# Optimization experiments

Measured on AMD Instinct MI355X. Metric: run time of the kernel, lower is better.

The kernel has to match this reference:

```python
import jax, jax.numpy as jnp
import numpy as np

B, T_IN, H, IN, OUT, T_DEC = 32768, 20, 128, 2, 2, 45


def lstm_cell(x, h, c, Wih, Whh, bih, bhh):
    # PyTorch gate order: i, f, g, o
    gates = x @ Wih.T + h @ Whh.T + (bih + bhh)
    i, f, g, o = jnp.split(gates, 4, axis=-1)
    c = jax.nn.sigmoid(f) * c + jax.nn.sigmoid(i) * jnp.tanh(g)
    h = jax.nn.sigmoid(o) * jnp.tanh(c)
    return h, c


def lstm_layer(xs, Wih, Whh, bih, bhh):
    # xs: [T, B, in] -> outputs [T, B, H], final (h, c)
    Bsz = xs.shape[1]
    h0 = jnp.zeros((Bsz, H), xs.dtype)
    c0 = jnp.zeros((Bsz, H), xs.dtype)

    def step(carry, x):
        h, c = carry
        h, c = lstm_cell(x, h, c, Wih, Whh, bih, bhh)
        return (h, c), h

    (h, c), ys = jax.lax.scan(step, (h0, c0), xs)
    return ys, h, c


def setup_inputs() -> dict:
    key = jax.random.key(0)
    ks = jax.random.split(key, 20)
    s = 0.05
    d = {
        'input_seq': jax.random.normal(ks[0], (B, T_IN, IN), jnp.float32),
        'enc_Wih0': jax.random.normal(ks[1], (4 * H, IN), jnp.float32) * s,
        'enc_Whh0': jax.random.normal(ks[2], (4 * H, H), jnp.float32) * s,
        'enc_bih0': jax.random.normal(ks[3], (4 * H,), jnp.float32) * s,
        'enc_bhh0': jax.random.normal(ks[4], (4 * H,), jnp.float32) * s,
        'enc_Wih1': jax.random.normal(ks[5], (4 * H, H), jnp.float32) * s,
        'enc_Whh1': jax.random.normal(ks[6], (4 * H, H), jnp.float32) * s,
        'enc_bih1': jax.random.normal(ks[7], (4 * H,), jnp.float32) * s,
        'enc_bhh1': jax.random.normal(ks[8], (4 * H,), jnp.float32) * s,
        'dec_Wih0': jax.random.normal(ks[9], (4 * H, OUT), jnp.float32) * s,
        'dec_Whh0': jax.random.normal(ks[10], (4 * H, H), jnp.float32) * s,
        'dec_bih0': jax.random.normal(ks[11], (4 * H,), jnp.float32) * s,
        'dec_bhh0': jax.random.normal(ks[12], (4 * H,), jnp.float32) * s,
        'dec_Wih1': jax.random.normal(ks[13], (4 * H, H), jnp.float32) * s,
        'dec_Whh1': jax.random.normal(ks[14], (4 * H, H), jnp.float32) * s,
        'dec_bih1': jax.random.normal(ks[15], (4 * H,), jnp.float32) * s,
        'dec_bhh1': jax.random.normal(ks[16], (4 * H,), jnp.float32) * s,
        'fc_W': jax.random.normal(ks[17], (OUT, H), jnp.float32) * s,
        'fc_b': jax.random.normal(ks[18], (OUT,), jnp.float32) * s,
        'target_len': T_DEC,
    }
    return d


def reference(input_seq, enc_Wih0, enc_Whh0, enc_bih0, enc_bhh0,
              enc_Wih1, enc_Whh1, enc_bih1, enc_bhh1,
              dec_Wih0, dec_Whh0, dec_bih0, dec_bhh0,
              dec_Wih1, dec_Whh1, dec_bih1, dec_bhh1,
              fc_W, fc_b, target_len):
    xs = jnp.swapaxes(input_seq, 0, 1)  # [T, B, IN]
    # Encoder: 2 stacked LSTM layers; keep final (h, c) of each layer.
    ys0, h0, c0 = lstm_layer(xs, enc_Wih0, enc_Whh0, enc_bih0, enc_bhh0)
    _, h1, c1 = lstm_layer(ys0, enc_Wih1, enc_Whh1, enc_bih1, enc_bhh1)

    x0 = input_seq[:, -1, :]  # [B, OUT] last observed point

    def dec_step(carry, _):
        hh0, cc0, hh1, cc1, x = carry
        hh0, cc0 = lstm_cell(x, hh0, cc0, dec_Wih0, dec_Whh0, dec_bih0, dec_bhh0)
        hh1, cc1 = lstm_cell(hh0, hh1, cc1, dec_Wih1, dec_Whh1, dec_bih1, dec_bhh1)
        pred = hh1 @ fc_W.T + fc_b  # [B, OUT]
        return (hh0, cc0, hh1, cc1, pred), pred

    _, preds = jax.lax.scan(dec_step, (h0, c0, h1, c1, x0), None, length=target_len)
    return jnp.swapaxes(preds, 0, 1)  # [B, target_len, OUT]
```

## Files before the change

### kernel.cpp

```cpp
#include <hip/hip_runtime.h>

typedef unsigned int u32;
typedef unsigned short u16;
typedef __attribute__((ext_vector_type(8))) short short8;
typedef __attribute__((ext_vector_type(4))) float floatx4;

#define L2E  1.44269504088896340736f
#define L2E2 2.88539008177792681472f

static __device__ __forceinline__ u16 f2bf(float f){
  u32 u = __float_as_uint(f);
  u = (u + 0x7FFFu + ((u >> 16) & 1u)) >> 16;
  return (u16)u;
}
static __device__ __forceinline__ u32 pk2bf(float lo, float hi){
  u32 r; asm("v_cvt_pk_bf16_f32 %0, %1, %2" : "=v"(r) : "v"(lo), "v"(hi)); return r;
}
static __device__ __forceinline__ float rcp_(float x){ return __builtin_amdgcn_rcpf(x); }
static __device__ __forceinline__ float exp2_(float x){ return __builtin_amdgcn_exp2f(x); }
static __device__ __forceinline__ float sigm2(float yh){ return rcp_(1.f + exp2_(-yh)); }
static __device__ __forceinline__ float tanh2(float yh2){ return 1.f - 2.f*rcp_(1.f + exp2_(yh2)); }

__global__ __launch_bounds__(256) void prep_weights(
    const float* eWhh0, const float* eWhh1, const float* eWih1,
    const float* dWhh0, const float* dWhh1, const float* dWih1,
    u16* wE0, u16* wE1h, u16* wE1x, u16* wD0, u16* wD1h, u16* wD1x)
{
  int idx = blockIdx.x * 256 + threadIdx.x;
  int m = idx >> 16, e = idx & 65535;
  int j = e & 7, L = (e >> 3) & 63, c = (e >> 9) & 3, g = (e >> 11) & 3, s = (e >> 13) & 7;
  int row = g*128 + s*16 + (L & 15);
  int col = c*32 + ((L >> 4) * 8) + j;
  float scale = (g == 2) ? L2E2 : L2E;
  const float* src; u16* dst;
  switch(m){
    case 0: src = eWhh0; dst = wE0;  break;
    case 1: src = eWhh1; dst = wE1h; break;
    case 2: src = eWih1; dst = wE1x; break;
    case 3: src = dWhh0; dst = wD0;  break;
    case 4: src = dWhh1; dst = wD1h; break;
    default:src = dWih1; dst = wD1x; break;
  }
  dst[e] = f2bf(src[row*128 + col] * scale);
}

__global__ __launch_bounds__(256) void prep_small(
    const float* ebih0,const float* ebhh0,const float* ebih1,const float* ebhh1,
    const float* dbih0,const float* dbhh0,const float* dbih1,const float* dbhh1,
    const float* eWih0,const float* dWih0, float* biasAll, float* wxAll)
{
  int i = blockIdx.x*256 + threadIdx.x;
  if (i < 2048){
    int l = i >> 9, n = i & 511, g = (n >> 7) & 3;
    const float* a = l==0?ebih0: l==1?ebih1: l==2?dbih0: dbih1;
    const float* b = l==0?ebhh0: l==1?ebhh1: l==2?dbhh0: dbhh1;
    biasAll[i] = (a[n] + b[n]) * ((g==2)? L2E2 : L2E);
  } else {
    int k = i - 2048;
    int l = k >> 10, e2 = k & 1023, n = e2 >> 1, g = (n >> 7) & 3;
    const float* wsrc = l ? dWih0 : eWih0;
    wxAll[k] = wsrc[e2] * ((g==2)? L2E2 : L2E);
  }
}

static __device__ __forceinline__ void stage_unit(
    const u16* __restrict__ s0, const u16* __restrict__ s1, u16* dst, int tid)
{
  const int off = tid * 16;
  char* d = (char*)dst;
  const char* a = (const char*)s0;
  const char* b = (const char*)s1;
  __builtin_amdgcn_global_load_lds((__attribute__((address_space(1))) void*)(a + off),
                                   (__attribute__((address_space(3))) void*)(d + off), 16, 0, 0);
  __builtin_amdgcn_global_load_lds((__attribute__((address_space(1))) void*)(a + 8192 + off),
                                   (__attribute__((address_space(3))) void*)(d + 8192 + off), 16, 0, 0);
  __builtin_amdgcn_global_load_lds((__attribute__((address_space(1))) void*)(b + off),
                                   (__attribute__((address_space(3))) void*)(d + 16384 + off), 16, 0, 0);
  __builtin_amdgcn_global_load_lds((__attribute__((address_space(1))) void*)(b + 8192 + off),
                                   (__attribute__((address_space(3))) void*)(d + 24576 + off), 16, 0, 0);
}

template<bool DEC>
static __device__ __forceinline__ void step_t(
    int grp, int mtb, int lane, int n4, int q, int m0, int t, int tid,
    u16* h0s, u16* h1s, u16 (*stg)[16384], float* fcp,
    const float* sB, const float* sWx, const float* sFc,
    const u16* __restrict__ W0, const u16* __restrict__ W1h,
    const u16* __restrict__ W1x, const u16* __restrict__ W0next,
    short8 (&ah)[2][4], float2 (&xc)[2][4],
    floatx4 (&c0a)[2][4], floatx4 (&c1a)[2][4],
    float* __restrict__ out)
{
  const int bofs = DEC ? 1024 : 0;
  const int wxo  = DEC ? 512  : 0;
  const int lb = lane * 8;
  const int grpo = grp * 8192;

  short8 a1[2][4];
  #pragma unroll
  for (int j = 0; j < 2; j++)
    #pragma unroll
    for (int c = 0; c < 4; c++)
      a1[j][c] = *(const short8*)(h1s + ((mtb+j)*4 + c)*512 + lb);

  #pragma unroll 1
  for (int i = 0; i < 4; i++){
    const int s = grp*4 + i;
    if (i < 3) stage_unit(W0 + (i+1)*8192, W0 + (5+i)*8192, stg[(i+1)&1], tid);
    else       stage_unit(W1h, W1h + 4*8192, stg[0], tid);
    const u16* bs = stg[i&1] + grpo;
    short8 bw[16];
    #pragma unroll
    for (int k = 0; k < 16; k++)
      bw[k] = *(const short8*)(bs + k*512 + lb);
    floatx4 acc[4][2];
    #pragma unroll
    for (int g = 0; g < 4; g++){
      float bi = sB[bofs + g*128 + s*16 + n4];
      float2 wv = ((const float2*)sWx)[wxo + g*128 + s*16 + n4];
      #pragma unroll
      for (int j = 0; j < 2; j++)
        #pragma unroll
        for (int r = 0; r < 4; r++)
          acc[g][j][r] = fmaf(xc[j][r].y, wv.y, fmaf(xc[j][r].x, wv.x, bi));
    }
    #pragma unroll
    for (int c = 0; c < 4; c++)
      #pragma unroll
      for (int g = 0; g < 4; g++){
        acc[g][0] = __builtin_amdgcn_mfma_f32_16x16x32_bf16(ah[0][c], bw[g*4+c], acc[g][0], 0,0,0);
        acc[g][1] = __builtin_amdgcn_mfma_f32_16x16x32_bf16(ah[1][c], bw[g*4+c], acc[g][1], 0,0,0);
      }
    #pragma unroll
    for (int j = 0; j < 2; j++){
      const int hb = ((mtb+j)*4 + (s>>1))*512 + ((s&1)*2 + (n4>>3))*128 + q*32 + (n4&7);
      floatx4 cc = c0a[j][i], cn;
      float hv[4];
      #pragma unroll
      for (int r = 0; r < 4; r++){
        float ig = sigm2(acc[0][j][r]);
        float fg = sigm2(acc[1][j][r]);
        float gg = tanh2(acc[2][j][r]);
        float cv = fmaf(fg, cc[r], ig*gg);
        float og = sigm2(acc[3][j][r]);
        hv[r] = og * (1.f - 2.f*rcp_(1.f + exp2_(L2E2*cv)));
        cn[r] = cv;
      }
      u32 p01 = pk2bf(hv[0], hv[1]), p23 = pk2bf(hv[2], hv[3]);
      h0s[hb +  0] = (u16)p01;
      h0s[hb +  8] = (u16)(p01 >> 16);
      h0s[hb + 16] = (u16)p23;
      h0s[hb + 24] = (u16)(p23 >> 16);
      c0a[j][i] = cn;
    }
    __syncthreads();
  }

  #pragma unroll
  for (int j = 0; j < 2; j++)
    #pragma unroll
    for (int c = 0; c < 4; c++)
      ah[j][c] = *(const short8*)(h0s + ((mtb+j)*4 + c)*512 + lb);

  float p[2][4][2];
  if (DEC){
    #pragma unroll
    for (int j = 0; j < 2; j++)
      #pragma unroll
      for (int r = 0; r < 4; r++){ p[j][r][0] = 0.f; p[j][r][1] = 0.f; }
  }

  #pragma unroll 1
  for (int i = 0; i < 4; i++){
    const int s = grp*4 + i;
    floatx4 acc[4][2];
    {
      stage_unit(W1x + i*8192, W1x + (4+i)*8192, stg[1], tid);
      const u16* bs = stg[0] + grpo;
      short8 bw[16];
      #pragma unroll
      for (int k = 0; k < 16; k++)
        bw[k] = *(const short8*)(bs + k*512 + lb);
      #pragma unroll
      for (int g = 0; g < 4; g++){
        float bi = sB[bofs + 512 + g*128 + s*16 + n4];
        #pragma unroll
        for (int j = 0; j < 2; j++)
          #pragma unroll
          for (int r = 0; r < 4; r++) acc[g][j][r] = bi;
      }
      #pragma unroll
      for (int c = 0; c < 4; c++)
        #pragma unroll
        for (int g = 0; g < 4; g++){
          acc[g][0] = __builtin_amdgcn_mfma_f32_16x16x32_bf16(a1[0][c], bw[g*4+c], acc[g][0], 0,0,0);
          acc[g][1] = __builtin_amdgcn_mfma_f32_16x16x32_bf16(a1[1][c], bw[g*4+c], acc[g][1], 0,0,0);
        }
      __syncthreads();
    }
    {
      if (i < 3)        stage_unit(W1h + (i+1)*8192, W1h + (5+i)*8192, stg[0], tid);
      else if (W0next)  stage_unit(W0next, W0next + 4*8192, stg[0], tid);
      const u16* bs = stg[1] + grpo;
      short8 bw[16];
      #pragma unroll
      for (int k = 0; k < 16; k++)
        bw[k] = *(const short8*)(bs + k*512 + lb);
      #pragma unroll
      for (int c = 0; c < 4; c++)
        #pragma unroll
        for (int g = 0; g < 4; g++){
          acc[g][0] = __builtin_amdgcn_mfma_f32_16x16x32_bf16(ah[0][c], bw[g*4+c], acc[g][0], 0,0,0);
          acc[g][1] = __builtin_amdgcn_mfma_f32_16x16x32_bf16(ah[1][c], bw[g*4+c], acc[g][1], 0,0,0);
        }
    }
    float f0 = 0.f, f1 = 0.f;
    if (DEC){ f0 = sFc[s*16 + n4]; f1 = sFc[128 + s*16 + n4]; }
    #pragma unroll
    for (int j = 0; j < 2; j++){
      const int hb = ((mtb+j)*4 + (s>>1))*512 + ((s&1)*2 + (n4>>3))*128 + q*32 + (n4&7);
      floatx4 cc = c1a[j][i], cn;
      float hv[4];
      #pragma unroll
      for (int r = 0; r < 4; r++){
        float ig = sigm2(acc[0][j][r]);
        float fg = sigm2(acc[1][j][r]);
        float gg = tanh2(acc[2][j][r]);
        float cv = fmaf(fg, cc[r], ig*gg);
        float og = sigm2(acc[3][j][r]);
        hv[r] = og * (1.f - 2.f*rcp_(1.f + exp2_(L2E2*cv)));
        cn[r] = cv;
        if (DEC){
          p[j][r][0] = fmaf(hv[r], f0, p[j][r][0]);
          p[j][r][1] = fmaf(hv[r], f1, p[j][r][1]);
        }
      }
      u32 p01 = pk2bf(hv[0], hv[1]), p23 = pk2bf(hv[2], hv[3]);
      h1s[hb +  0] = (u16)p01;
      h1s[hb +  8] = (u16)(p01 >> 16);
      h1s[hb + 16] = (u16)p23;
      h1s[hb + 24] = (u16)(p23 >> 16);
      c1a[j][i] = cn;
    }
    if (DEC && i == 3){
      #pragma unroll
      for (int off = 1; off < 16; off <<= 1)
        #pragma unroll
        for (int j = 0; j < 2; j++)
          #pragma unroll
          for (int r = 0; r < 4; r++){
            p[j][r][0] += __shfl_xor(p[j][r][0], off);
            p[j][r][1] += __shfl_xor(p[j][r][1], off);
          }
      if (n4 == 0){
        #pragma unroll
        for (int j = 0; j < 2; j++)
          #pragma unroll
          for (int r = 0; r < 4; r++){
            const int base = ((mtb+j)*16 + q*4 + r)*4 + grp*2;
            fcp[base + 0] = p[j][r][0];
            fcp[base + 1] = p[j][r][1];
          }
      }
    }
    __syncthreads();
  }

  if (DEC){
    const float fb0 = sFc[256], fb1 = sFc[257];
    #pragma unroll
    for (int j = 0; j < 2; j++)
      #pragma unroll
      for (int r = 0; r < 4; r++){
        const int base = ((mtb+j)*16 + q*4 + r)*4;
        float2 pv;
        pv.x = fcp[base + 0] + fcp[base + 2] + fb0;
        pv.y = fcp[base + 1] + fcp[base + 3] + fb1;
        xc[j][r] = pv;
        if (grp == 0 && n4 == 0)
          *(float2*)(out + (long)(m0 + (mtb+j)*16 + q*4 + r)*90 + (t - 20)*2) = pv;
      }
  }
}

__global__ __launch_bounds__(512, 1) void lstm_all(
    const float* __restrict__ in_seq,
    const u16* __restrict__ wE0, const u16* __restrict__ wE1h, const u16* __restrict__ wE1x,
    const u16* __restrict__ wD0, const u16* __restrict__ wD1h, const u16* __restrict__ wD1x,
    const float* __restrict__ biasAll, const float* __restrict__ wxAll,
    const float* __restrict__ fcW, const float* __restrict__ fcb,
    float* __restrict__ out)
{
  __shared__ u16 h0s[16384];
  __shared__ u16 h1s[16384];
  __shared__ u16 stg[2][16384];
  __shared__ float sB[2048];
  __shared__ float sWx[2048];
  __shared__ float sFc[260];
  __shared__ float fcp[512];

  const int tid = threadIdx.x, lane = tid & 63, w = tid >> 6;
  const int grp = w >> 2, mtb = (w & 3) * 2;
  const int n4 = lane & 15, q = lane >> 4;
  const int m0 = blockIdx.x * 128;

  for (int i = tid; i < 2048; i += 512){ sB[i] = biasAll[i]; sWx[i] = wxAll[i]; }
  if (tid < 258) sFc[tid] = (tid < 256) ? fcW[tid] : fcb[tid - 256];
  { u32* z0 = (u32*)h0s; u32* z1 = (u32*)h1s;
    for (int i = tid; i < 8192; i += 512){ z0[i] = 0u; z1[i] = 0u; } }

  floatx4 c0a[2][4], c1a[2][4];
  const floatx4 z4 = {0.f,0.f,0.f,0.f};
  #pragma unroll
  for (int j = 0; j < 2; j++)
    #pragma unroll
    for (int i = 0; i < 4; i++){ c0a[j][i] = z4; c1a[j][i] = z4; }

  stage_unit(wE0, wE0 + 4*8192, stg[0], tid);
  __syncthreads();

  short8 ah[2][4];
  #pragma unroll
  for (int j = 0; j < 2; j++)
    #pragma unroll
    for (int c = 0; c < 4; c++)
      ah[j][c] = *(const short8*)(h0s + ((mtb+j)*4 + c)*512 + lane*8);
  __syncthreads();

  float2 xc[2][4];

  #pragma unroll 1
  for (int t = 0; t < 20; t++){
    #pragma unroll
    for (int j = 0; j < 2; j++)
      #pragma unroll
      for (int r = 0; r < 4; r++)
        xc[j][r] = *(const float2*)(in_seq + (long)(m0 + (mtb+j)*16 + q*4 + r)*40 + t*2);
    step_t<false>(grp, mtb, lane, n4, q, m0, t, tid, h0s, h1s, stg, fcp,
                  sB, sWx, sFc, wE0, wE1h, wE1x, (t < 19) ? wE0 : wD0,
                  ah, xc, c0a, c1a, out);
  }

  #pragma unroll
  for (int j = 0; j < 2; j++)
    #pragma unroll
    for (int r = 0; r < 4; r++)
      xc[j][r] = *(const float2*)(in_seq + (long)(m0 + (mtb+j)*16 + q*4 + r)*40 + 38);

  #pragma unroll 1
  for (int t = 20; t < 65; t++){
    step_t<true>(grp, mtb, lane, n4, q, m0, t, tid, h0s, h1s, stg, fcp,
                 sB, sWx, sFc, wD0, wD1h, wD1x, (t < 64) ? wD0 : (const u16*)nullptr,
                 ah, xc, c0a, c1a, out);
  }
}

extern "C" void kernel_launch(void* const* d_in, const int* in_sizes, int n_in,
                              void* d_out, int out_size, void* d_ws, size_t ws_size,
                              hipStream_t stream)
{
  const float* in_seq = (const float*)d_in[0];
  const float* eWih0 = (const float*)d_in[1];
  const float* eWhh0 = (const float*)d_in[2];
  const float* ebih0 = (const float*)d_in[3];
  const float* ebhh0 = (const float*)d_in[4];
  const float* eWih1 = (const float*)d_in[5];
  const float* eWhh1 = (const float*)d_in[6];
  const float* ebih1 = (const float*)d_in[7];
  const float* ebhh1 = (const float*)d_in[8];
  const float* dWih0 = (const float*)d_in[9];
  const float* dWhh0 = (const float*)d_in[10];
  const float* dbih0 = (const float*)d_in[11];
  const float* dbhh0 = (const float*)d_in[12];
  const float* dWih1 = (const float*)d_in[13];
  const float* dWhh1 = (const float*)d_in[14];
  const float* dbih1 = (const float*)d_in[15];
  const float* dbhh1 = (const float*)d_in[16];
  const float* fcW   = (const float*)d_in[17];
  const float* fcb   = (const float*)d_in[18];
  float* out = (float*)d_out;
  char* ws = (char*)d_ws;

  u16* wE0   = (u16*)(ws + 0);
  u16* wE1h  = (u16*)(ws + 131072);
  u16* wE1x  = (u16*)(ws + 262144);
  u16* wD0   = (u16*)(ws + 393216);
  u16* wD1h  = (u16*)(ws + 524288);
  u16* wD1x  = (u16*)(ws + 655360);
  float* biasAll = (float*)(ws + 786432);
  float* wxAll   = (float*)(ws + 794624);

  hipLaunchKernelGGL(prep_weights, dim3(1536), dim3(256), 0, stream,
                     eWhh0, eWhh1, eWih1, dWhh0, dWhh1, dWih1,
                     wE0, wE1h, wE1x, wD0, wD1h, wD1x);
  hipLaunchKernelGGL(prep_small, dim3(16), dim3(256), 0, stream,
                     ebih0, ebhh0, ebih1, ebhh1, dbih0, dbhh0, dbih1, dbhh1,
                     eWih0, dWih0, biasAll, wxAll);

  hipLaunchKernelGGL(lstm_all, dim3(256), dim3(512), 0, stream,
                     in_seq, (const u16*)wE0, (const u16*)wE1h, (const u16*)wE1x,
                     (const u16*)wD0, (const u16*)wD1h, (const u16*)wD1x,
                     (const float*)biasAll, (const float*)wxAll, fcW, fcb, out);
}
```

Before: 1.524 ms.

## Replace block barriers and LDS weight staging with pairwise wave flags and direct loads

```diff
diff --git a/kernel.cpp b/kernel.cpp
--- a/kernel.cpp
+++ b/kernel.cpp
@@ -63,30 +63,23 @@
   }
 }
 
-static __device__ __forceinline__ void stage_unit(
-    const u16* __restrict__ s0, const u16* __restrict__ s1, u16* dst, int tid)
-{
-  const int off = tid * 16;
-  char* d = (char*)dst;
-  const char* a = (const char*)s0;
-  const char* b = (const char*)s1;
-  __builtin_amdgcn_global_load_lds((__attribute__((address_space(1))) void*)(a + off),
-                                   (__attribute__((address_space(3))) void*)(d + off), 16, 0, 0);
-  __builtin_amdgcn_global_load_lds((__attribute__((address_space(1))) void*)(a + 8192 + off),
-                                   (__attribute__((address_space(3))) void*)(d + 8192 + off), 16, 0, 0);
-  __builtin_amdgcn_global_load_lds((__attribute__((address_space(1))) void*)(b + off),
-                                   (__attribute__((address_space(3))) void*)(d + 16384 + off), 16, 0, 0);
-  __builtin_amdgcn_global_load_lds((__attribute__((address_space(1))) void*)(b + 8192 + off),
-                                   (__attribute__((address_space(3))) void*)(d + 24576 + off), 16, 0, 0);
+static __device__ __forceinline__ void pair_sync(
+    volatile int* sig, int w, int wp, int e, int lane)
+{
+  asm volatile("s_waitcnt lgkmcnt(0)" ::: "memory");
+  if (lane == 0) sig[w] = e;
+  while (sig[wp] < e) __builtin_amdgcn_s_sleep(2);
+  asm volatile("" ::: "memory");
+  __builtin_amdgcn_sched_barrier(0);
 }
 
 template<bool DEC>
 static __device__ __forceinline__ void step_t(
-    int grp, int mtb, int lane, int n4, int q, int m0, int t, int tid,
-    u16* h0s, u16* h1s, u16 (*stg)[16384], float* fcp,
+    int w, int wp, int grp, int mtb, int lane, int n4, int q, int m0, int t,
+    u16* h0s, u16* h1s, float* fcp, volatile int* sig0, volatile int* sig1,
     const float* sB, const float* sWx, const float* sFc,
     const u16* __restrict__ W0, const u16* __restrict__ W1h,
-    const u16* __restrict__ W1x, const u16* __restrict__ W0next,
+    const u16* __restrict__ W1x,
     short8 (&ah)[2][4], float2 (&xc)[2][4],
     floatx4 (&c0a)[2][4], floatx4 (&c1a)[2][4],
     float* __restrict__ out)
@@ -94,7 +87,7 @@
   const int bofs = DEC ? 1024 : 0;
   const int wxo  = DEC ? 512  : 0;
   const int lb = lane * 8;
-  const int grpo = grp * 8192;
+  const int epoch = t + 1;
 
   short8 a1[2][4];
   #pragma unroll
@@ -106,9 +99,7 @@
   #pragma unroll 1
   for (int i = 0; i < 4; i++){
     const int s = grp*4 + i;
-    if (i < 3) stage_unit(W0 + (i+1)*8192, W0 + (5+i)*8192, stg[(i+1)&1], tid);
-    else       stage_unit(W1h, W1h + 4*8192, stg[0], tid);
-    const u16* bs = stg[i&1] + grpo;
+    const u16* bs = W0 + s*8192;
     short8 bw[16];
     #pragma unroll
     for (int k = 0; k < 16; k++)
@@ -124,6 +115,7 @@
         for (int r = 0; r < 4; r++)
           acc[g][j][r] = fmaf(xc[j][r].y, wv.y, fmaf(xc[j][r].x, wv.x, bi));
     }
+    __builtin_amdgcn_s_setprio(1);
     #pragma unroll
     for (int c = 0; c < 4; c++)
       #pragma unroll
@@ -131,6 +123,7 @@
         acc[g][0] = __builtin_amdgcn_mfma_f32_16x16x32_bf16(ah[0][c], bw[g*4+c], acc[g][0], 0,0,0);
         acc[g][1] = __builtin_amdgcn_mfma_f32_16x16x32_bf16(ah[1][c], bw[g*4+c], acc[g][1], 0,0,0);
       }
+    __builtin_amdgcn_s_setprio(0);
     #pragma unroll
     for (int j = 0; j < 2; j++){
       const int hb = ((mtb+j)*4 + (s>>1))*512 + ((s&1)*2 + (n4>>3))*128 + q*32 + (n4&7);
@@ -153,8 +146,8 @@
       h0s[hb + 24] = (u16)(p23 >> 16);
       c0a[j][i] = cn;
     }
-    __syncthreads();
-  }
+  }
+  pair_sync(sig0, w, wp, epoch, lane);
 
   #pragma unroll
   for (int j = 0; j < 2; j++)
@@ -174,21 +167,21 @@
   for (int i = 0; i < 4; i++){
     const int s = grp*4 + i;
     floatx4 acc[4][2];
+    #pragma unroll
+    for (int g = 0; g < 4; g++){
+      float bi = sB[bofs + 512 + g*128 + s*16 + n4];
+      #pragma unroll
+      for (int j = 0; j < 2; j++)
+        #pragma unroll
+        for (int r = 0; r < 4; r++) acc[g][j][r] = bi;
+    }
     {
-      stage_unit(W1x + i*8192, W1x + (4+i)*8192, stg[1], tid);
-      const u16* bs = stg[0] + grpo;
+      const u16* bs = W1h + s*8192;
       short8 bw[16];
       #pragma unroll
       for (int k = 0; k < 16; k++)
         bw[k] = *(const short8*)(bs + k*512 + lb);
-      #pragma unroll
-      for (int g = 0; g < 4; g++){
-        float bi = sB[bofs + 512 + g*128 + s*16 + n4];
-        #pragma unroll
-        for (int j = 0; j < 2; j++)
-          #pragma unroll
-          for (int r = 0; r < 4; r++) acc[g][j][r] = bi;
-      }
+      __builtin_amdgcn_s_setprio(1);
       #pragma unroll
       for (int c = 0; c < 4; c++)
         #pragma unroll
@@ -196,16 +189,15 @@
           acc[g][0] = __builtin_amdgcn_mfma_f32_16x16x32_bf16(a1[0][c], bw[g*4+c], acc[g][0], 0,0,0);
           acc[g][1] = __builtin_amdgcn_mfma_f32_16x16x32_bf16(a1[1][c], bw[g*4+c], acc[g][1], 0,0,0);
         }
-      __syncthreads();
+      __builtin_amdgcn_s_setprio(0);
     }
     {
-      if (i < 3)        stage_unit(W1h + (i+1)*8192, W1h + (5+i)*8192, stg[0], tid);
-      else if (W0next)  stage_unit(W0next, W0next + 4*8192, stg[0], tid);
-      const u16* bs = stg[1] + grpo;
+      const u16* bs = W1x + s*8192;
       short8 bw[16];
       #pragma unroll
       for (int k = 0; k < 16; k++)
         bw[k] = *(const short8*)(bs + k*512 + lb);
+      __builtin_amdgcn_s_setprio(1);
       #pragma unroll
       for (int c = 0; c < 4; c++)
         #pragma unroll
@@ -213,6 +205,7 @@
           acc[g][0] = __builtin_amdgcn_mfma_f32_16x16x32_bf16(ah[0][c], bw[g*4+c], acc[g][0], 0,0,0);
           acc[g][1] = __builtin_amdgcn_mfma_f32_16x16x32_bf16(ah[1][c], bw[g*4+c], acc[g][1], 0,0,0);
         }
+      __builtin_amdgcn_s_setprio(0);
     }
     float f0 = 0.f, f1 = 0.f;
     if (DEC){ f0 = sFc[s*16 + n4]; f1 = sFc[128 + s*16 + n4]; }
@@ -242,29 +235,30 @@
       h1s[hb + 24] = (u16)(p23 >> 16);
       c1a[j][i] = cn;
     }
-    if (DEC && i == 3){
-      #pragma unroll
-      for (int off = 1; off < 16; off <<= 1)
-        #pragma unroll
-        for (int j = 0; j < 2; j++)
-          #pragma unroll
-          for (int r = 0; r < 4; r++){
-            p[j][r][0] += __shfl_xor(p[j][r][0], off);
-            p[j][r][1] += __shfl_xor(p[j][r][1], off);
-          }
-      if (n4 == 0){
-        #pragma unroll
-        for (int j = 0; j < 2; j++)
-          #pragma unroll
-          for (int r = 0; r < 4; r++){
-            const int base = ((mtb+j)*16 + q*4 + r)*4 + grp*2;
-            fcp[base + 0] = p[j][r][0];
-            fcp[base + 1] = p[j][r][1];
-          }
-      }
-    }
-    __syncthreads();
-  }
+  }
+
+  if (DEC){
+    #pragma unroll
+    for (int off = 1; off < 16; off <<= 1)
+      #pragma unroll
+      for (int j = 0; j < 2; j++)
+        #pragma unroll
+        for (int r = 0; r < 4; r++){
+          p[j][r][0] += __shfl_xor(p[j][r][0], off);
+          p[j][r][1] += __shfl_xor(p[j][r][1], off);
+        }
+    if (n4 == 0){
+      #pragma unroll
+      for (int j = 0; j < 2; j++)
+        #pragma unroll
+        for (int r = 0; r < 4; r++){
+          const int base = ((mtb+j)*16 + q*4 + r)*4 + grp*2;
+          fcp[base + 0] = p[j][r][0];
+          fcp[base + 1] = p[j][r][1];
+        }
+    }
+  }
+  pair_sync(sig1, w, wp, epoch, lane);
 
   if (DEC){
     const float fb0 = sFc[256], fb1 = sFc[257];
@@ -293,19 +287,21 @@
 {
   __shared__ u16 h0s[16384];
   __shared__ u16 h1s[16384];
-  __shared__ u16 stg[2][16384];
   __shared__ float sB[2048];
   __shared__ float sWx[2048];
   __shared__ float sFc[260];
   __shared__ float fcp[512];
+  __shared__ int  sig[16];
 
   const int tid = threadIdx.x, lane = tid & 63, w = tid >> 6;
+  const int wp = w ^ 4;
   const int grp = w >> 2, mtb = (w & 3) * 2;
   const int n4 = lane & 15, q = lane >> 4;
   const int m0 = blockIdx.x * 128;
 
   for (int i = tid; i < 2048; i += 512){ sB[i] = biasAll[i]; sWx[i] = wxAll[i]; }
   if (tid < 258) sFc[tid] = (tid < 256) ? fcW[tid] : fcb[tid - 256];
+  if (tid < 16) sig[tid] = 0;
   { u32* z0 = (u32*)h0s; u32* z1 = (u32*)h1s;
     for (int i = tid; i < 8192; i += 512){ z0[i] = 0u; z1[i] = 0u; } }
 
@@ -315,8 +311,6 @@
   for (int j = 0; j < 2; j++)
     #pragma unroll
     for (int i = 0; i < 4; i++){ c0a[j][i] = z4; c1a[j][i] = z4; }
-
-  stage_unit(wE0, wE0 + 4*8192, stg[0], tid);
   __syncthreads();
 
   short8 ah[2][4];
@@ -336,9 +330,9 @@
       #pragma unroll
       for (int r = 0; r < 4; r++)
         xc[j][r] = *(const float2*)(in_seq + (long)(m0 + (mtb+j)*16 + q*4 + r)*40 + t*2);
-    step_t<false>(grp, mtb, lane, n4, q, m0, t, tid, h0s, h1s, stg, fcp,
-                  sB, sWx, sFc, wE0, wE1h, wE1x, (t < 19) ? wE0 : wD0,
-                  ah, xc, c0a, c1a, out);
+    step_t<false>(w, wp, grp, mtb, lane, n4, q, m0, t, h0s, h1s, fcp,
+                  sig, sig + 8, sB, sWx, sFc,
+                  wE0, wE1h, wE1x, ah, xc, c0a, c1a, out);
   }
 
   #pragma unroll
@@ -349,9 +343,9 @@
 
   #pragma unroll 1
   for (int t = 20; t < 65; t++){
-    step_t<true>(grp, mtb, lane, n4, q, m0, t, tid, h0s, h1s, stg, fcp,
-                 sB, sWx, sFc, wD0, wD1h, wD1x, (t < 64) ? wD0 : (const u16*)nullptr,
-                 ah, xc, c0a, c1a, out);
+    step_t<true>(w, wp, grp, mtb, lane, n4, q, m0, t, h0s, h1s, fcp,
+                 sig, sig + 8, sB, sWx, sFc,
+                 wD0, wD1h, wD1x, ah, xc, c0a, c1a, out);
   }
 }
 
```

Result: faster. 1.400 ms (-8.1%).
